# Kernel tuning notes

Hardware: AMD Instinct MI355X
Metric: run time of the kernel (lower is better)

The kernel has to match this reference:

```python
import jax, jax.numpy as jnp
import numpy as np

N_CAT, N_NUM, N_EMB, N_ENG = 53, 47, 1352, 100
E, H, FF, NEXP, NL = 128, 4, 256, 5, 6
B, L = 512, 51
EPS = 1e-5

def _ln(x, w, b):
    m = jnp.mean(x, axis=-1, keepdims=True)
    v = jnp.mean((x - m) ** 2, axis=-1, keepdims=True)
    return (x - m) * jax.lax.rsqrt(v + EPS) * w + b

def setup_inputs() -> dict:
    key = jax.random.key(0)
    ks = jax.random.split(key, 24)
    s = 0.02
    emb = jax.random.normal(ks[0], (N_EMB + 2, E), jnp.float32) * s
    emb = emb.at[0].set(0.0)  # padding_idx=0
    emb_eng = jax.random.normal(ks[1], (N_ENG, E), jnp.float32) * s
    emb_eng = emb_eng.at[0].set(0.0)
    inp = {
        'x_cat': jax.random.randint(ks[2], (B, L, N_CAT), 0, 1306, jnp.int32),
        'x_num': jax.random.normal(ks[3], (B, L, N_NUM), jnp.float32),
        'x_engineered': jax.random.normal(ks[4], (B, N_ENG), jnp.float32),
        'emb': emb,
        'emb_bias': jax.random.normal(ks[5], (N_CAT + N_NUM, E), jnp.float32),
        'emb_eng': emb_eng,
        'emb_bias_eng': jax.random.normal(ks[6], (N_ENG, E), jnp.float32),
        'ln0_w': jnp.ones((E,), jnp.float32), 'ln0_b': jnp.zeros((E,), jnp.float32),
        'ln1_w': jnp.ones((NL, E), jnp.float32), 'ln1_b': jnp.zeros((NL, E), jnp.float32),
        'Wqkv': jax.random.normal(ks[7], (NL, 3 * E, E), jnp.float32) * s,
        'bqkv': jnp.zeros((NL, 3 * E), jnp.float32),
        'Wo': jax.random.normal(ks[8], (NL, E, E), jnp.float32) * s,
        'bo': jnp.zeros((NL, E), jnp.float32),
        'ln2_w': jnp.ones((NL, E), jnp.float32), 'ln2_b': jnp.zeros((NL, E), jnp.float32),
        'Wg': jax.random.normal(ks[9], (NL, E, NEXP), jnp.float32) * s,
        'bg': jnp.zeros((NL, NEXP), jnp.float32),
        'W1': jax.random.normal(ks[10], (NL, NEXP, E, FF), jnp.float32) * s,
        'b1': jnp.zeros((NL, NEXP, FF), jnp.float32),
        'W2': jax.random.normal(ks[11], (NL, NEXP, FF, E), jnp.float32) * s,
        'b2': jnp.zeros((NL, NEXP, E), jnp.float32),
    }
    return inp

def _forward(x_cat, x_num, x_engineered, emb, emb_bias, emb_eng, emb_bias_eng,
             ln0_w, ln0_b, ln1_w, ln1_b, Wqkv, bqkv, Wo, bo,
             ln2_w, ln2_b, Wg, bg, W1, b1, W2, b2):
    b = x_cat.shape[0]
    # last order
    cat_last = x_cat[:, -1, :]                     # [B, N_CAT]
    num_last = x_num[:, -1, :]                     # [B, N_NUM]
    x_cat_emb = emb[cat_last] + emb_bias[:N_CAT][None]          # [B, N_CAT, E]
    num_idx = jnp.arange(N_EMB - N_NUM + 1, N_EMB + 1)           # rows 1306..1352
    x_num_emb = emb[num_idx][None] * num_last[..., None] + emb_bias[N_CAT:][None]
    eng_emb = emb_eng[None] * x_engineered[..., None] + emb_bias_eng[None]
    dummy = jnp.zeros((b, 1, E), x_cat_emb.dtype)
    x = jnp.concatenate([x_cat_emb, x_num_emb, eng_emb, dummy], axis=1)  # [B, 201, E]
    x = _ln(x, ln0_w, ln0_b)
    hd = E // H
    scale = 1.0 / np.sqrt(hd)
    for i in range(NL):
        # pre-norm multi-head self-attention
        h = _ln(x, ln1_w[i], ln1_b[i])
        qkv = h @ Wqkv[i].T + bqkv[i]              # [B, N, 3E]
        q, k, v = jnp.split(qkv, 3, axis=-1)
        q = q.reshape(b, -1, H, hd); k = k.reshape(b, -1, H, hd); v = v.reshape(b, -1, H, hd)
        scores = jnp.einsum('bqhd,bkhd->bhqk', q, k) * scale
        attn = jax.nn.softmax(scores, axis=-1)
        o = jnp.einsum('bhqk,bkhd->bqhd', attn, v).reshape(b, -1, E)
        x = x + o @ Wo[i].T + bo[i]
        # pre-norm MoE feedforward (dense soft mixture over experts)
        h = _ln(x, ln2_w[i], ln2_b[i])
        gate = jax.nn.softmax(h @ Wg[i] + bg[i], axis=-1)        # [B, N, NEXP]
        hid = jax.nn.relu(jnp.einsum('bne,xef->bnxf', h, W1[i]) + b1[i])
        eo = jnp.einsum('bnxf,xfe->bnxe', hid, W2[i]) + b2[i]
        x = x + jnp.einsum('bnxe,bnx->bne', eo, gate)
    return x[:, -1, :]                              # [B, E]

def reference(x_cat, x_num, x_engineered, emb, emb_bias, emb_eng, emb_bias_eng,
              ln0_w, ln0_b, ln1_w, ln1_b, Wqkv, bqkv, Wo, bo,
              ln2_w, ln2_b, Wg, bg, W1, b1, W2, b2):
    return _forward(x_cat, x_num, x_engineered, emb, emb_bias, emb_eng, emb_bias_eng,
                    ln0_w, ln0_b, ln1_w, ln1_b, Wqkv, bqkv, Wo, bo,
                    ln2_w, ln2_b, Wg, bg, W1, b1, W2, b2)
```

## Files before the change

### kernel.cpp

```cpp
#include <hip/hip_runtime.h>
#include <math.h>

#define NTOK 201
#define EDIM 128
#define LDX  132
#define NHEAD 4
#define HD   32
#define NLAY 6
#define NEXP 5
#define FFD  256
#define NCAT 53
#define NNUM 47
#define NENG 100
#define NEMB 1352
#define SEQL 51
#define NB   512
#define LN_EPS 1e-5f
#define SCALE 0.17677669529663687f

typedef __attribute__((ext_vector_type(8))) short bfrag;
typedef __attribute__((ext_vector_type(4))) float f32x4;
typedef __attribute__((ext_vector_type(8))) unsigned short u16x8;
typedef __attribute__((ext_vector_type(4))) unsigned short u16x4;

__device__ __forceinline__ float bf2f(unsigned short u){ return __uint_as_float(((unsigned)u)<<16); }
__device__ __forceinline__ unsigned short f2bf(float f){
  unsigned u = __float_as_uint(f);
  return (unsigned short)((u + 0x7FFFu + ((u>>16)&1u)) >> 16);
}

#define OFF_WQH  0u
#define OFF_WQL  589824u
#define OFF_BQ   1179648u
#define OFF_WOH  1188864u
#define OFF_WOL  1385472u
#define OFF_W1H  1582080u
#define OFF_W1L  3548160u
#define OFF_W2H  5514240u
#define OFF_W2L  7480320u

__global__ void prep_qkv_bf(const float* __restrict__ Wqkv, const float* __restrict__ bqkv,
                            unsigned short* __restrict__ Wqh, unsigned short* __restrict__ Wql,
                            float* __restrict__ bq){
  int bid = blockIdx.x; int n = bid % 384; int e = threadIdx.x;
  float sc = (n < 128) ? SCALE : 1.0f;
  float w = Wqkv[(size_t)bid*128 + e] * sc;
  unsigned short h = f2bf(w), l = f2bf(w - bf2f(h));
  Wqh[(size_t)bid*128 + e] = h; Wql[(size_t)bid*128 + e] = l;
  if (e == 0) bq[bid] = bqkv[bid] * sc;
}

__global__ void prep_wo_bf(const float* __restrict__ Wo,
                           unsigned short* __restrict__ Woh, unsigned short* __restrict__ Wol){
  int idx = blockIdx.x*blockDim.x + threadIdx.x;
  if (idx >= 6*128*128) return;
  float w = Wo[idx];
  unsigned short h = f2bf(w), l = f2bf(w - bf2f(h));
  Woh[idx] = h; Wol[idx] = l;
}

__global__ void prep_moe(const float* __restrict__ W1, const float* __restrict__ W2,
                         unsigned short* __restrict__ W1h, unsigned short* __restrict__ W1l,
                         unsigned short* __restrict__ W2h, unsigned short* __restrict__ W2l){
  const int Ntot = 6*5*128*256;
  for (int idx = blockIdx.x*blockDim.x + threadIdx.x; idx < Ntot; idx += gridDim.x*blockDim.x){
    int lx = idx / 32768; int rem = idx & 32767; int e = rem >> 8; int f = rem & 255;
    float w = W1[idx];
    unsigned short h = f2bf(w); unsigned short l = f2bf(w - bf2f(h));
    size_t o1 = (size_t)(lx*256+f)*128 + e;
    W1h[o1] = h; W1l[o1] = l;
    int f2 = (idx >> 7) & 255; int e2 = idx & 127;
    float w2 = W2[idx];
    unsigned short h2 = f2bf(w2); unsigned short l2 = f2bf(w2 - bf2f(h2));
    size_t o2 = (size_t)(lx*128+e2)*256 + f2;
    W2h[o2] = h2; W2l[o2] = l2;
  }
}

struct Params {
  const int*   x_cat;
  const float* x_num;
  const float* x_eng;
  const float* emb;
  const float* emb_bias;
  const float* emb_eng;
  const float* emb_bias_eng;
  const float* ln0w; const float* ln0b;
  const float* ln1w; const float* ln1b;
  const float* ln2w; const float* ln2b;
  const float* bo;
  const float* Wg;   const float* bg;
  const float* b1;   const float* b2;
  const unsigned short* Wqh; const unsigned short* Wql; const float* bq;
  const unsigned short* Woh; const unsigned short* Wol;
  const unsigned short* W1h; const unsigned short* W1l;
  const unsigned short* W2h; const unsigned short* W2l;
  float* out;
};

__device__ __forceinline__ void ln_stats(const float* xs, float* s_m, float* s_r, int tid){
  if (tid < NTOK){
    const float* row = xs + tid*LDX;
    float s0=0,s1=0,s2=0,s3=0;
    for (int e=0;e<EDIM;e+=4){ s0+=row[e]; s1+=row[e+1]; s2+=row[e+2]; s3+=row[e+3]; }
    float m = (s0+s1+s2+s3)*(1.0f/EDIM);
    float v0=0,v1=0,v2=0,v3=0;
    for (int e=0;e<EDIM;e+=4){
      float d0=row[e]-m,d1=row[e+1]-m,d2=row[e+2]-m,d3=row[e+3]-m;
      v0+=d0*d0; v1+=d1*d1; v2+=d2*d2; v3+=d3*d3;
    }
    s_m[tid]=m; s_r[tid]=1.0f/sqrtf((v0+v1+v2+v3)*(1.0f/EDIM)+LN_EPS);
  }
}

__global__ __launch_bounds__(512) __attribute__((amdgpu_waves_per_eu(2,2)))
void fam_fwd(Params p){
  __shared__ float xs[NTOK*LDX];
  __shared__ float s_m[NTOK], s_r[NTOK];
  __shared__ __align__(16) char scb[55296];

  const int b = blockIdx.x, tid = threadIdx.x;
  const int lane = tid & 63, wv = tid >> 6;

  {
    const int e = tid & 127, tl = tid >> 7;
    for (int t = tl; t < NTOK; t += 4){
      float v;
      if (t < NCAT){
        int idx = p.x_cat[b*(SEQL*NCAT) + (SEQL-1)*NCAT + t];
        v = p.emb[idx*EDIM+e] + p.emb_bias[t*EDIM+e];
      } else if (t < NCAT+NNUM){
        int j = t - NCAT;
        float nv = p.x_num[b*(SEQL*NNUM)+(SEQL-1)*NNUM+j];
        v = p.emb[(NEMB-NNUM+1+j)*EDIM+e]*nv + p.emb_bias[(NCAT+j)*EDIM+e];
      } else if (t < NCAT+NNUM+NENG){
        int j = t - (NCAT+NNUM);
        float ev = p.x_eng[b*NENG+j];
        v = p.emb_eng[j*EDIM+e]*ev + p.emb_bias_eng[j*EDIM+e];
      } else v = 0.f;
      xs[t*LDX+e] = v;
    }
  }
  __syncthreads();
  ln_stats(xs, s_m, s_r, tid);
  __syncthreads();
  {
    const int e = tid & 127, tl = tid >> 7;
    for (int t = tl; t < NTOK; t += 4){
      float m = s_m[t], r = s_r[t];
      xs[t*LDX+e] = (xs[t*LDX+e]-m)*r*p.ln0w[e] + p.ln0b[e];
    }
  }
  __syncthreads();

  unsigned short* Kh  = (unsigned short*)scb;
  unsigned short* Vt  = (unsigned short*)(scb + 17920);
  unsigned short* HTh = (unsigned short*)(scb + 32768);
  unsigned short* HTl = (unsigned short*)(scb + 32768 + 8704);
  unsigned short* Sb  = (unsigned short*)(scb + 32768);
  unsigned short* Ob  = (unsigned short*)(scb + 32768 + 14848);
  unsigned short* Qmh = (unsigned short*)(scb + 50176);
  unsigned short* Qml = (unsigned short*)(scb + 52736);
  float* red  = (float*)(scb + 52736);
  float* mrow = (float*)(scb + 52736 + 1056);
  float* dsum = (float*)(scb + 52736 + 1184);
  unsigned short* Ahi = (unsigned short*)scb;
  unsigned short* Alo = (unsigned short*)(scb + 8192);
  unsigned short* Hh  = (unsigned short*)(scb + 16384);
  unsigned short* Hl  = (unsigned short*)(scb + 32768);
  float*          gateb = (float*)(scb + 49152);

  for (int li = 0; li < NLAY; ++li){
    const float* ln1w = p.ln1w + li*EDIM;
    const float* ln1b = p.ln1b + li*EDIM;
    const float* ln2w = p.ln2w + li*EDIM;
    const float* ln2b = p.ln2b + li*EDIM;
    const float* bo   = p.bo + li*EDIM;
    const float* Wg   = p.Wg + li*EDIM*NEXP;
    const float* bg   = p.bg + li*NEXP;
    const float* b1g  = p.b1 + li*NEXP*FFD;
    const float* b2g  = p.b2 + li*NEXP*EDIM;

    ln_stats(xs, s_m, s_r, tid);
    __syncthreads();

    f32x4 accW[7][2];
#pragma unroll
    for (int mt=0; mt<7; ++mt){ accW[mt][0]=(f32x4){0,0,0,0}; accW[mt][1]=(f32x4){0,0,0,0}; }

    const int mfw = wv & 1;
    const int ngw = wv >> 1;

    for (int h = 0; h < NHEAD; ++h){
      {
        int sel = ngw;
        int nrow = ((sel < 2) ? (128 + h*HD + sel*16) : (256 + h*HD + (sel-2)*16)) + (lane & 15);
        const unsigned short* Bh = p.Wqh + ((size_t)li*384 + nrow)*128 + 8*(lane>>4);
        const unsigned short* Bl = p.Wql + ((size_t)li*384 + nrow)*128 + 8*(lane>>4);
        bfrag wbh[4], wbl[4];
#pragma unroll
        for (int kf=0; kf<4; ++kf){ wbh[kf] = *(const bfrag*)(Bh + kf*32); wbl[kf] = *(const bfrag*)(Bl + kf*32); }
        float bias = p.bq[li*384 + nrow];

        for (int mt=0; mt<7; ++mt){
          {
            int row = tid >> 4, c8 = (tid & 15) << 3;
            int t = mt*32 + row;
            union { unsigned short u[8]; u16x8 v; } hu, lu;
            if (t < NTOK){
              float m = s_m[t], r = s_r[t];
              const float* xr = &xs[t*LDX + c8];
              float4 a = *(const float4*)xr, b4 = *(const float4*)(xr+4);
              float4 w0 = *(const float4*)(ln1w + c8), w1 = *(const float4*)(ln1w + c8 + 4);
              float4 q0 = *(const float4*)(ln1b + c8), q1 = *(const float4*)(ln1b + c8 + 4);
              float vv[8] = {(a.x-m)*r*w0.x+q0.x,(a.y-m)*r*w0.y+q0.y,(a.z-m)*r*w0.z+q0.z,(a.w-m)*r*w0.w+q0.w,
                             (b4.x-m)*r*w1.x+q1.x,(b4.y-m)*r*w1.y+q1.y,(b4.z-m)*r*w1.z+q1.z,(b4.w-m)*r*w1.w+q1.w};
#pragma unroll
              for (int j2=0;j2<8;++j2){ unsigned short hb=f2bf(vv[j2]); hu.u[j2]=hb; lu.u[j2]=f2bf(vv[j2]-bf2f(hb)); }
            } else {
#pragma unroll
              for (int j2=0;j2<8;++j2){ hu.u[j2]=0; lu.u[j2]=0; }
            }
            *(u16x8*)(HTh + row*136 + c8) = hu.v;
            *(u16x8*)(HTl + row*136 + c8) = lu.v;
          }
          __syncthreads();
          {
            f32x4 acc = (f32x4){0,0,0,0};
#pragma unroll
            for (int kf=0; kf<4; ++kf){
              const unsigned short* ab = HTh + (mfw*16 + (lane&15))*136 + kf*32 + 8*(lane>>4);
              const unsigned short* al = HTl + (mfw*16 + (lane&15))*136 + kf*32 + 8*(lane>>4);
              bfrag ah = *(const bfrag*)ab, av = *(const bfrag*)al;
              acc = __builtin_amdgcn_mfma_f32_16x16x32_bf16(ah, wbh[kf], acc, 0,0,0);
              acc = __builtin_amdgcn_mfma_f32_16x16x32_bf16(ah, wbl[kf], acc, 0,0,0);
              acc = __builtin_amdgcn_mfma_f32_16x16x32_bf16(av, wbh[kf], acc, 0,0,0);
            }
            int col = lane & 15;
            if (sel < 2){
              int d = sel*16 + col;
#pragma unroll
              for (int reg=0; reg<4; ++reg){
                int tok = mt*32 + mfw*16 + 4*(lane>>4) + reg;
                Kh[tok*40 + d] = f2bf(acc[reg] + bias);
              }
            } else {
              int d = (sel-2)*16 + col;
              int tokb = mt*32 + mfw*16 + 4*(lane>>4);
              u16x4 pk;
#pragma unroll
              for (int reg=0; reg<4; ++reg) pk[reg] = f2bf(acc[reg] + bias);
              *(u16x4*)(Vt + d*232 + tokb) = pk;
            }
          }
          __syncthreads();
        }
      }

      bfrag wobh[2], wobl[2];
#pragma unroll
      for (int i=0;i<2;++i){
        int j = (ngw + 4*i)*16 + (lane&15);
        const unsigned short* wb = p.Woh + ((size_t)li*128 + j)*128 + h*HD + 8*(lane>>4);
        const unsigned short* wl = p.Wol + ((size_t)li*128 + j)*128 + h*HD + 8*(lane>>4);
        wobh[i] = *(const bfrag*)wb; wobl[i] = *(const bfrag*)wl;
      }

#pragma unroll
      for (int mt=0; mt<7; ++mt){
        {
          int row = tid >> 4, c8 = (tid & 15) << 3;
          int t = mt*32 + row;
          union { unsigned short u[8]; u16x8 v; } hu, lu;
          if (t < NTOK){
            float m = s_m[t], r = s_r[t];
            const float* xr = &xs[t*LDX + c8];
            float4 a = *(const float4*)xr, b4 = *(const float4*)(xr+4);
            float4 w0 = *(const float4*)(ln1w + c8), w1 = *(const float4*)(ln1w + c8 + 4);
            float4 q0 = *(const float4*)(ln1b + c8), q1 = *(const float4*)(ln1b + c8 + 4);
            float vv[8] = {(a.x-m)*r*w0.x+q0.x,(a.y-m)*r*w0.y+q0.y,(a.z-m)*r*w0.z+q0.z,(a.w-m)*r*w0.w+q0.w,
                           (b4.x-m)*r*w1.x+q1.x,(b4.y-m)*r*w1.y+q1.y,(b4.z-m)*r*w1.z+q1.z,(b4.w-m)*r*w1.w+q1.w};
#pragma unroll
            for (int j2=0;j2<8;++j2){ unsigned short hb=f2bf(vv[j2]); hu.u[j2]=hb; lu.u[j2]=f2bf(vv[j2]-bf2f(hb)); }
          } else {
#pragma unroll
            for (int j2=0;j2<8;++j2){ hu.u[j2]=0; lu.u[j2]=0; }
          }
          *(u16x8*)(HTh + row*136 + c8) = hu.v;
          *(u16x8*)(HTl + row*136 + c8) = lu.v;
        }
        __syncthreads();

        if (wv < 4){
          int mf2 = wv & 1, nf = (wv >> 1) & 1;
          int nrow = h*HD + nf*16 + (lane & 15);
          const unsigned short* Bh = p.Wqh + ((size_t)li*384 + nrow)*128 + 8*(lane>>4);
          const unsigned short* Bl = p.Wql + ((size_t)li*384 + nrow)*128 + 8*(lane>>4);
          f32x4 acc = (f32x4){0,0,0,0};
#pragma unroll
          for (int kf=0; kf<4; ++kf){
            bfrag ah = *(const bfrag*)(HTh + (mf2*16 + (lane&15))*136 + kf*32 + 8*(lane>>4));
            bfrag av = *(const bfrag*)(HTl + (mf2*16 + (lane&15))*136 + kf*32 + 8*(lane>>4));
            bfrag bh = *(const bfrag*)(Bh + kf*32);
            bfrag bl = *(const bfrag*)(Bl + kf*32);
            acc = __builtin_amdgcn_mfma_f32_16x16x32_bf16(ah, bh, acc, 0,0,0);
            acc = __builtin_amdgcn_mfma_f32_16x16x32_bf16(ah, bl, acc, 0,0,0);
            acc = __builtin_amdgcn_mfma_f32_16x16x32_bf16(av, bh, acc, 0,0,0);
          }
          float bias = p.bq[li*384 + nrow];
          int d = nf*16 + (lane & 15);
#pragma unroll
          for (int reg=0; reg<4; ++reg){
            float v = acc[reg] + bias;
            unsigned short hb = f2bf(v);
            int qrow = mf2*16 + 4*(lane>>4) + reg;
            Qmh[qrow*40 + d] = hb;
            Qml[qrow*40 + d] = f2bf(v - bf2f(hb));
          }
        }
        __syncthreads();

        {
          bfrag qh = *(const bfrag*)(Qmh + (mfw*16 + (lane&15))*40 + 8*(lane>>4));
          bfrag ql = *(const bfrag*)(Qml + (mfw*16 + (lane&15))*40 + 8*(lane>>4));
          for (int nf = ngw; nf < 14; nf += 4){
            bfrag kb = *(const bfrag*)(Kh + (nf*16 + (lane&15))*40 + 8*(lane>>4));
            f32x4 s = (f32x4){0,0,0,0};
            s = __builtin_amdgcn_mfma_f32_16x16x32_bf16(qh, kb, s, 0,0,0);
            s = __builtin_amdgcn_mfma_f32_16x16x32_bf16(ql, kb, s, 0,0,0);
            int tok = nf*16 + (lane & 15);
#pragma unroll
            for (int reg=0; reg<4; ++reg){
              int q = mfw*16 + 4*(lane>>4) + reg;
              Sb[q*232 + tok] = f2bf(s[reg]);
            }
          }
        }
        __syncthreads();

        {
          int q = tid & 31, kg = tid >> 5;
          float pmax = -INFINITY;
#pragma unroll
          for (int j2=0; j2<14; ++j2){
            int k = kg + 16*j2;
            if (k < NTOK) pmax = fmaxf(pmax, bf2f(Sb[q*232 + k]));
          }
          pmax = fmaxf(pmax, __shfl_xor(pmax, 32));
          if (!(tid & 32)) red[(tid>>6)*33 + q] = pmax;
        }
        __syncthreads();
        if (tid < 32){
          float m = red[tid];
#pragma unroll
          for (int w=1; w<8; ++w) m = fmaxf(m, red[w*33 + tid]);
          mrow[tid] = m;
        }
        __syncthreads();

        {
          int q = tid & 31, kg = tid >> 5;
          float mr = mrow[q];
          float psum = 0.f;
#pragma unroll
          for (int j2=0; j2<14; ++j2){
            int k = kg + 16*j2;
            float pe = 0.f;
            if (k < NTOK) pe = __expf(bf2f(Sb[q*232 + k]) - mr);
            psum += pe;
            Sb[q*232 + k] = f2bf(pe);
          }
          psum += __shfl_xor(psum, 32);
          if (!(tid & 32)) red[(tid>>6)*33 + q] = psum;
        }
        __syncthreads();
        if (tid < 32){
          float s = red[tid];
#pragma unroll
          for (int w=1; w<8; ++w) s += red[w*33 + tid];
          dsum[tid] = s;
        }
        __syncthreads();

        if (wv < 4){
          int mf2 = wv & 1, nf = (wv >> 1) & 1;
          f32x4 o = (f32x4){0,0,0,0};
#pragma unroll
          for (int kf=0; kf<7; ++kf){
            bfrag pa = *(const bfrag*)(Sb + (mf2*16 + (lane&15))*232 + kf*32 + 8*(lane>>4));
            bfrag vb = *(const bfrag*)(Vt + (nf*16 + (lane&15))*232 + kf*32 + 8*(lane>>4));
            o = __builtin_amdgcn_mfma_f32_16x16x32_bf16(pa, vb, o, 0,0,0);
          }
          int d = nf*16 + (lane & 15);
#pragma unroll
          for (int reg=0; reg<4; ++reg){
            int q = mf2*16 + 4*(lane>>4) + reg;
            Ob[q*40 + d] = f2bf(o[reg] * (1.0f/dsum[q]));
          }
        }
        __syncthreads();

        {
          bfrag oa = *(const bfrag*)(Ob + (mfw*16 + (lane&15))*40 + 8*(lane>>4));
          accW[mt][0] = __builtin_amdgcn_mfma_f32_16x16x32_bf16(oa, wobh[0], accW[mt][0], 0,0,0);
          accW[mt][0] = __builtin_amdgcn_mfma_f32_16x16x32_bf16(oa, wobl[0], accW[mt][0], 0,0,0);
          accW[mt][1] = __builtin_amdgcn_mfma_f32_16x16x32_bf16(oa, wobh[1], accW[mt][1], 0,0,0);
          accW[mt][1] = __builtin_amdgcn_mfma_f32_16x16x32_bf16(oa, wobl[1], accW[mt][1], 0,0,0);
        }
        __syncthreads();
      }
    }

    {
#pragma unroll
      for (int i=0;i<2;++i){
        int j = (ngw + 4*i)*16 + (lane & 15);
        float boj = bo[j];
#pragma unroll
        for (int mt=0; mt<7; ++mt){
#pragma unroll
          for (int reg=0; reg<4; ++reg){
            int t = mt*32 + mfw*16 + 4*(lane>>4) + reg;
            if (t < NTOK) xs[t*LDX + j] += accW[mt][i][reg] + boj;
          }
        }
      }
    }
    __syncthreads();

    ln_stats(xs, s_m, s_r, tid);
    __syncthreads();

    if (tid < NTOK){
      const float* row = xs + tid*LDX;
      float m = s_m[tid], r = s_r[tid];
      float gl[NEXP];
#pragma unroll
      for (int x=0;x<NEXP;++x) gl[x] = bg[x];
      for (int e=0;e<EDIM;++e){
        float hv = (row[e]-m)*r*ln2w[e] + ln2b[e];
#pragma unroll
        for (int x=0;x<NEXP;++x) gl[x] += hv*Wg[e*NEXP+x];
      }
      float gm = gl[0];
#pragma unroll
      for (int x=1;x<NEXP;++x) gm = fmaxf(gm, gl[x]);
      float gs = 0.f;
#pragma unroll
      for (int x=0;x<NEXP;++x){ gl[x] = __expf(gl[x]-gm); gs += gl[x]; }
      float gi = 1.0f/gs;
#pragma unroll
      for (int x=0;x<NEXP;++x) gateb[tid*NEXP+x] = gl[x]*gi;
    }
    __syncthreads();

    for (int t0 = 0; t0 < NTOK; t0 += 32){
      {
        int mf = tid >> 8;
        int row = (tid & 15) + 16*mf;
        int kb  = ((tid>>6)&3)*32 + 8*((tid>>4)&3);
        int t = t0 + row;
        union { unsigned short u[8]; bfrag v; } hu, lu;
        if (t < NTOK){
          float m = s_m[t], r = s_r[t];
          const float* xr = &xs[t*LDX + kb];
          float4 a = *(const float4*)xr;
          float4 bq4 = *(const float4*)(xr+4);
          float4 w0 = *(const float4*)(ln2w + kb);
          float4 w1 = *(const float4*)(ln2w + kb + 4);
          float4 bb0 = *(const float4*)(ln2b + kb);
          float4 bb1 = *(const float4*)(ln2b + kb + 4);
          float vv[8] = {(a.x-m)*r*w0.x+bb0.x, (a.y-m)*r*w0.y+bb0.y,
                         (a.z-m)*r*w0.z+bb0.z, (a.w-m)*r*w0.w+bb0.w,
                         (bq4.x-m)*r*w1.x+bb1.x, (bq4.y-m)*r*w1.y+bb1.y,
                         (bq4.z-m)*r*w1.z+bb1.z, (bq4.w-m)*r*w1.w+bb1.w};
#pragma unroll
          for (int j=0;j<8;++j){
            unsigned short hb = f2bf(vv[j]);
            hu.u[j] = hb;
            lu.u[j] = f2bf(vv[j] - bf2f(hb));
          }
        } else {
#pragma unroll
          for (int j=0;j<8;++j){ hu.u[j]=0; lu.u[j]=0; }
        }
        *(bfrag*)(Ahi + tid*8) = hu.v;
        *(bfrag*)(Alo + tid*8) = lu.v;
      }
      __syncthreads();

      f32x4 acc2[2];
      acc2[0] = (f32x4){0.f,0.f,0.f,0.f};
      acc2[1] = (f32x4){0.f,0.f,0.f,0.f};

      for (int x = 0; x < NEXP; ++x){
        const unsigned short* W1hx = p.W1h + (size_t)(li*NEXP+x)*FFD*EDIM;
        const unsigned short* W1lx = p.W1l + (size_t)(li*NEXP+x)*FFD*EDIM;
        const unsigned short* W2hx = p.W2h + (size_t)(li*NEXP+x)*EDIM*FFD;
        const unsigned short* W2lx = p.W2l + (size_t)(li*NEXP+x)*EDIM*FFD;

        f32x4 acc1[2][2];
#pragma unroll
        for (int i=0;i<2;++i){ acc1[i][0]=(f32x4){0,0,0,0}; acc1[i][1]=(f32x4){0,0,0,0}; }
#pragma unroll
        for (int kf=0;kf<4;++kf){
          bfrag ah[2], al[2], bh[2], bl[2];
#pragma unroll
          for (int mf=0;mf<2;++mf){
            ah[mf] = *(const bfrag*)(Ahi + ((mf*4+kf)*64 + lane)*8);
            al[mf] = *(const bfrag*)(Alo + ((mf*4+kf)*64 + lane)*8);
          }
#pragma unroll
          for (int nfl=0;nfl<2;++nfl){
            size_t n = (size_t)((wv*2+nfl)*16 + (lane&15));
            size_t off = n*128 + kf*32 + 8*(lane>>4);
            bh[nfl] = *(const bfrag*)(W1hx + off);
            bl[nfl] = *(const bfrag*)(W1lx + off);
          }
#pragma unroll
          for (int mf=0;mf<2;++mf)
#pragma unroll
            for (int nfl=0;nfl<2;++nfl){
              acc1[mf][nfl] = __builtin_amdgcn_mfma_f32_16x16x32_bf16(ah[mf], bh[nfl], acc1[mf][nfl], 0,0,0);
              acc1[mf][nfl] = __builtin_amdgcn_mfma_f32_16x16x32_bf16(ah[mf], bl[nfl], acc1[mf][nfl], 0,0,0);
              acc1[mf][nfl] = __builtin_amdgcn_mfma_f32_16x16x32_bf16(al[mf], bh[nfl], acc1[mf][nfl], 0,0,0);
            }
        }
        {
          int c = lane & 15;
#pragma unroll
          for (int nfl=0;nfl<2;++nfl){
            int n = (wv*2+nfl)*16 + c;
            float bb = b1g[x*FFD + n];
            int lane_t_base = 16*(2*nfl + (c>>3));
            int jcol = c & 7;
#pragma unroll
            for (int mf=0;mf<2;++mf){
#pragma unroll
              for (int reg=0;reg<4;++reg){
                int msub = (lane>>4)*4 + reg;
                int t = t0 + mf*16 + msub;
                float g = (t < NTOK) ? gateb[t*NEXP+x] : 0.f;
                float v = fmaxf(acc1[mf][nfl][reg] + bb, 0.f) * g;
                unsigned short hb = f2bf(v);
                unsigned short lb = f2bf(v - bf2f(hb));
                int idx = ((mf*8 + wv)*64 + msub + lane_t_base)*8 + jcol;
                Hh[idx] = hb; Hl[idx] = lb;
              }
            }
          }
        }
        __syncthreads();

#pragma unroll
        for (int kf=0;kf<8;++kf){
          bfrag hh[2], hl[2];
#pragma unroll
          for (int mf=0;mf<2;++mf){
            hh[mf] = *(const bfrag*)(Hh + ((mf*8+kf)*64 + lane)*8);
            hl[mf] = *(const bfrag*)(Hl + ((mf*8+kf)*64 + lane)*8);
          }
          size_t off = (size_t)(wv*16 + (lane&15))*256 + kf*32 + 8*(lane>>4);
          bfrag wh = *(const bfrag*)(W2hx + off);
          bfrag wl = *(const bfrag*)(W2lx + off);
#pragma unroll
          for (int mf=0;mf<2;++mf){
            acc2[mf] = __builtin_amdgcn_mfma_f32_16x16x32_bf16(hh[mf], wh, acc2[mf], 0,0,0);
            acc2[mf] = __builtin_amdgcn_mfma_f32_16x16x32_bf16(hh[mf], wl, acc2[mf], 0,0,0);
            acc2[mf] = __builtin_amdgcn_mfma_f32_16x16x32_bf16(hl[mf], wh, acc2[mf], 0,0,0);
          }
        }
        __syncthreads();
      }

      {
        int c = lane & 15;
        int n = wv*16 + c;
#pragma unroll
        for (int mf=0;mf<2;++mf){
#pragma unroll
          for (int reg=0;reg<4;++reg){
            int t = t0 + mf*16 + (lane>>4)*4 + reg;
            if (t < NTOK){
              float bs = 0.f;
#pragma unroll
              for (int x=0;x<NEXP;++x) bs += gateb[t*NEXP+x]*b2g[x*EDIM+n];
              xs[t*LDX+n] += acc2[mf][reg] + bs;
            }
          }
        }
      }
      __syncthreads();
    }
  }

  if (tid < EDIM) p.out[b*EDIM + tid] = xs[200*LDX + tid];
}

extern "C" void kernel_launch(void* const* d_in, const int* in_sizes, int n_in,
                              void* d_out, int out_size, void* d_ws, size_t ws_size,
                              hipStream_t stream) {
  (void)in_sizes; (void)n_in; (void)out_size; (void)ws_size;
  char* ws = (char*)d_ws;

  const float* Wqkv = (const float*)d_in[11];
  const float* bqkv = (const float*)d_in[12];
  const float* Wo   = (const float*)d_in[13];
  const float* W1   = (const float*)d_in[19];
  const float* W2   = (const float*)d_in[21];

  hipLaunchKernelGGL(prep_qkv_bf, dim3(6*384), dim3(128), 0, stream,
                     Wqkv, bqkv,
                     (unsigned short*)(ws+OFF_WQH), (unsigned short*)(ws+OFF_WQL),
                     (float*)(ws+OFF_BQ));
  hipLaunchKernelGGL(prep_wo_bf, dim3(384), dim3(256), 0, stream, Wo,
                     (unsigned short*)(ws+OFF_WOH), (unsigned short*)(ws+OFF_WOL));
  hipLaunchKernelGGL(prep_moe, dim3(3840), dim3(256), 0, stream, W1, W2,
                     (unsigned short*)(ws+OFF_W1H), (unsigned short*)(ws+OFF_W1L),
                     (unsigned short*)(ws+OFF_W2H), (unsigned short*)(ws+OFF_W2L));

  Params p;
  p.x_cat        = (const int*)  d_in[0];
  p.x_num        = (const float*)d_in[1];
  p.x_eng        = (const float*)d_in[2];
  p.emb          = (const float*)d_in[3];
  p.emb_bias     = (const float*)d_in[4];
  p.emb_eng      = (const float*)d_in[5];
  p.emb_bias_eng = (const float*)d_in[6];
  p.ln0w = (const float*)d_in[7];  p.ln0b = (const float*)d_in[8];
  p.ln1w = (const float*)d_in[9];  p.ln1b = (const float*)d_in[10];
  p.ln2w = (const float*)d_in[15]; p.ln2b = (const float*)d_in[16];
  p.bo   = (const float*)d_in[14];
  p.Wg   = (const float*)d_in[17]; p.bg = (const float*)d_in[18];
  p.b1   = (const float*)d_in[20]; p.b2 = (const float*)d_in[22];
  p.Wqh = (const unsigned short*)(ws+OFF_WQH);
  p.Wql = (const unsigned short*)(ws+OFF_WQL);
  p.bq  = (const float*)(ws+OFF_BQ);
  p.Woh = (const unsigned short*)(ws+OFF_WOH);
  p.Wol = (const unsigned short*)(ws+OFF_WOL);
  p.W1h = (const unsigned short*)(ws+OFF_W1H);
  p.W1l = (const unsigned short*)(ws+OFF_W1L);
  p.W2h = (const unsigned short*)(ws+OFF_W2H);
  p.W2l = (const unsigned short*)(ws+OFF_W2L);
  p.out = (float*)d_out;

  hipLaunchKernelGGL(fam_fwd, dim3(NB), dim3(512), 0, stream, p);
}
```

Measured before the change: 5.539 ms.

## Double block size to 1024 threads and split MFMA accumulators for ILP

Launches 1024 threads per block (16 waves) instead of 512, redistributing QKV, attention, Wo and MoE FFN work so each wave handles fewer output tiles. It also splits each MFMA accumulation chain into two interleaved accumulators summed at the end, to shorten dependency chains. The aim is more latency hiding per block, given the LDS footprint limits blocks per CU. In exchange, register budget per thread shrinks, some phases leave half the waves idle (e.g. QKV and PV use only 8 or 4 waves), and block-wide barriers now synchronize more waves.

```diff
diff --git a/kernel.cpp b/kernel.cpp
--- a/kernel.cpp
+++ b/kernel.cpp
@@ -113,8 +113,31 @@
   }
 }
 
-__global__ __launch_bounds__(512) __attribute__((amdgpu_waves_per_eu(2,2)))
-void fam_fwd(Params p){
+__device__ __forceinline__ void stage_ht(const float* xs, const float* s_m, const float* s_r,
+                                         unsigned short* HTh, unsigned short* HTl,
+                                         const float* lw, const float* lb, int t0, int tid){
+  int row = tid >> 5;
+  int c4  = (tid & 31) << 2;
+  int t = t0 + row;
+  u16x4 hu = (u16x4){0,0,0,0}, lu = (u16x4){0,0,0,0};
+  if (t < NTOK){
+    float m = s_m[t], r = s_r[t];
+    float4 a  = *(const float4*)(&xs[t*LDX + c4]);
+    float4 w  = *(const float4*)(lw + c4);
+    float4 bb = *(const float4*)(lb + c4);
+    float v0 = (a.x-m)*r*w.x + bb.x;
+    float v1 = (a.y-m)*r*w.y + bb.y;
+    float v2 = (a.z-m)*r*w.z + bb.z;
+    float v3 = (a.w-m)*r*w.w + bb.w;
+    unsigned short h0=f2bf(v0), h1=f2bf(v1), h2=f2bf(v2), h3=f2bf(v3);
+    hu = (u16x4){h0,h1,h2,h3};
+    lu = (u16x4){f2bf(v0-bf2f(h0)), f2bf(v1-bf2f(h1)), f2bf(v2-bf2f(h2)), f2bf(v3-bf2f(h3))};
+  }
+  *(u16x4*)(HTh + row*136 + c4) = hu;
+  *(u16x4*)(HTl + row*136 + c4) = lu;
+}
+
+__global__ __launch_bounds__(1024, 4) void fam_fwd(Params p){
   __shared__ float xs[NTOK*LDX];
   __shared__ float s_m[NTOK], s_r[NTOK];
   __shared__ __align__(16) char scb[55296];
@@ -124,7 +147,7 @@
 
   {
     const int e = tid & 127, tl = tid >> 7;
-    for (int t = tl; t < NTOK; t += 4){
+    for (int t = tl; t < NTOK; t += 8){
       float v;
       if (t < NCAT){
         int idx = p.x_cat[b*(SEQL*NCAT) + (SEQL-1)*NCAT + t];
@@ -146,7 +169,7 @@
   __syncthreads();
   {
     const int e = tid & 127, tl = tid >> 7;
-    for (int t = tl; t < NTOK; t += 4){
+    for (int t = tl; t < NTOK; t += 8){
       float m = s_m[t], r = s_r[t];
       xs[t*LDX+e] = (xs[t*LDX+e]-m)*r*p.ln0w[e] + p.ln0b[e];
     }
@@ -162,8 +185,8 @@
   unsigned short* Qmh = (unsigned short*)(scb + 50176);
   unsigned short* Qml = (unsigned short*)(scb + 52736);
   float* red  = (float*)(scb + 52736);
-  float* mrow = (float*)(scb + 52736 + 1056);
-  float* dsum = (float*)(scb + 52736 + 1184);
+  float* mrow = (float*)(scb + 52736 + 2112);
+  float* dsum = (float*)(scb + 52736 + 2240);
   unsigned short* Ahi = (unsigned short*)scb;
   unsigned short* Alo = (unsigned short*)(scb + 8192);
   unsigned short* Hh  = (unsigned short*)(scb + 16384);
@@ -184,130 +207,103 @@
     ln_stats(xs, s_m, s_r, tid);
     __syncthreads();
 
-    f32x4 accW[7][2];
-#pragma unroll
-    for (int mt=0; mt<7; ++mt){ accW[mt][0]=(f32x4){0,0,0,0}; accW[mt][1]=(f32x4){0,0,0,0}; }
+    f32x4 accW[7];
+#pragma unroll
+    for (int mt=0; mt<7; ++mt) accW[mt]=(f32x4){0,0,0,0};
 
     const int mfw = wv & 1;
     const int ngw = wv >> 1;
 
     for (int h = 0; h < NHEAD; ++h){
-      {
-        int sel = ngw;
+      bfrag wbh[4], wbl[4]; float bias1 = 0.f;
+      if (wv < 8){
+        int sel = wv >> 1;
         int nrow = ((sel < 2) ? (128 + h*HD + sel*16) : (256 + h*HD + (sel-2)*16)) + (lane & 15);
         const unsigned short* Bh = p.Wqh + ((size_t)li*384 + nrow)*128 + 8*(lane>>4);
         const unsigned short* Bl = p.Wql + ((size_t)li*384 + nrow)*128 + 8*(lane>>4);
-        bfrag wbh[4], wbl[4];
 #pragma unroll
         for (int kf=0; kf<4; ++kf){ wbh[kf] = *(const bfrag*)(Bh + kf*32); wbl[kf] = *(const bfrag*)(Bl + kf*32); }
-        float bias = p.bq[li*384 + nrow];
-
-        for (int mt=0; mt<7; ++mt){
-          {
-            int row = tid >> 4, c8 = (tid & 15) << 3;
-            int t = mt*32 + row;
-            union { unsigned short u[8]; u16x8 v; } hu, lu;
-            if (t < NTOK){
-              float m = s_m[t], r = s_r[t];
-              const float* xr = &xs[t*LDX + c8];
-              float4 a = *(const float4*)xr, b4 = *(const float4*)(xr+4);
-              float4 w0 = *(const float4*)(ln1w + c8), w1 = *(const float4*)(ln1w + c8 + 4);
-              float4 q0 = *(const float4*)(ln1b + c8), q1 = *(const float4*)(ln1b + c8 + 4);
-              float vv[8] = {(a.x-m)*r*w0.x+q0.x,(a.y-m)*r*w0.y+q0.y,(a.z-m)*r*w0.z+q0.z,(a.w-m)*r*w0.w+q0.w,
-                             (b4.x-m)*r*w1.x+q1.x,(b4.y-m)*r*w1.y+q1.y,(b4.z-m)*r*w1.z+q1.z,(b4.w-m)*r*w1.w+q1.w};
-#pragma unroll
-              for (int j2=0;j2<8;++j2){ unsigned short hb=f2bf(vv[j2]); hu.u[j2]=hb; lu.u[j2]=f2bf(vv[j2]-bf2f(hb)); }
+        bias1 = p.bq[li*384 + nrow];
+      }
+
+      for (int mt=0; mt<7; ++mt){
+        stage_ht(xs, s_m, s_r, HTh, HTl, ln1w, ln1b, mt*32, tid);
+        __syncthreads();
+        if (wv < 8){
+          int sel = wv >> 1, mf1 = wv & 1;
+          f32x4 aA = (f32x4){0,0,0,0}, aB = (f32x4){0,0,0,0};
+#pragma unroll
+          for (int kf=0; kf<4; ++kf){
+            bfrag ah = *(const bfrag*)(HTh + (mf1*16 + (lane&15))*136 + kf*32 + 8*(lane>>4));
+            bfrag av = *(const bfrag*)(HTl + (mf1*16 + (lane&15))*136 + kf*32 + 8*(lane>>4));
+            if (kf & 1){
+              aB = __builtin_amdgcn_mfma_f32_16x16x32_bf16(ah, wbh[kf], aB, 0,0,0);
+              aB = __builtin_amdgcn_mfma_f32_16x16x32_bf16(ah, wbl[kf], aB, 0,0,0);
+              aB = __builtin_amdgcn_mfma_f32_16x16x32_bf16(av, wbh[kf], aB, 0,0,0);
             } else {
-#pragma unroll
-              for (int j2=0;j2<8;++j2){ hu.u[j2]=0; lu.u[j2]=0; }
+              aA = __builtin_amdgcn_mfma_f32_16x16x32_bf16(ah, wbh[kf], aA, 0,0,0);
+              aA = __builtin_amdgcn_mfma_f32_16x16x32_bf16(ah, wbl[kf], aA, 0,0,0);
+              aA = __builtin_amdgcn_mfma_f32_16x16x32_bf16(av, wbh[kf], aA, 0,0,0);
             }
-            *(u16x8*)(HTh + row*136 + c8) = hu.v;
-            *(u16x8*)(HTl + row*136 + c8) = lu.v;
-          }
-          __syncthreads();
-          {
-            f32x4 acc = (f32x4){0,0,0,0};
-#pragma unroll
-            for (int kf=0; kf<4; ++kf){
-              const unsigned short* ab = HTh + (mfw*16 + (lane&15))*136 + kf*32 + 8*(lane>>4);
-              const unsigned short* al = HTl + (mfw*16 + (lane&15))*136 + kf*32 + 8*(lane>>4);
-              bfrag ah = *(const bfrag*)ab, av = *(const bfrag*)al;
-              acc = __builtin_amdgcn_mfma_f32_16x16x32_bf16(ah, wbh[kf], acc, 0,0,0);
-              acc = __builtin_amdgcn_mfma_f32_16x16x32_bf16(ah, wbl[kf], acc, 0,0,0);
-              acc = __builtin_amdgcn_mfma_f32_16x16x32_bf16(av, wbh[kf], acc, 0,0,0);
+          }
+          f32x4 acc = aA + aB;
+          int col = lane & 15;
+          if (sel < 2){
+            int d = sel*16 + col;
+#pragma unroll
+            for (int reg=0; reg<4; ++reg){
+              int tok = mt*32 + mf1*16 + 4*(lane>>4) + reg;
+              Kh[tok*40 + d] = f2bf(acc[reg] + bias1);
             }
-            int col = lane & 15;
-            if (sel < 2){
-              int d = sel*16 + col;
-#pragma unroll
-              for (int reg=0; reg<4; ++reg){
-                int tok = mt*32 + mfw*16 + 4*(lane>>4) + reg;
-                Kh[tok*40 + d] = f2bf(acc[reg] + bias);
-              }
-            } else {
-              int d = (sel-2)*16 + col;
-              int tokb = mt*32 + mfw*16 + 4*(lane>>4);
-              u16x4 pk;
-#pragma unroll
-              for (int reg=0; reg<4; ++reg) pk[reg] = f2bf(acc[reg] + bias);
-              *(u16x4*)(Vt + d*232 + tokb) = pk;
-            }
-          }
-          __syncthreads();
-        }
-      }
-
-      bfrag wobh[2], wobl[2];
-#pragma unroll
-      for (int i=0;i<2;++i){
-        int j = (ngw + 4*i)*16 + (lane&15);
+          } else {
+            int d = (sel-2)*16 + col;
+            int tokb = mt*32 + mf1*16 + 4*(lane>>4);
+            u16x4 pk;
+#pragma unroll
+            for (int reg=0; reg<4; ++reg) pk[reg] = f2bf(acc[reg] + bias1);
+            *(u16x4*)(Vt + d*232 + tokb) = pk;
+          }
+        }
+        __syncthreads();
+      }
+
+      bfrag wobh, wobl;
+      {
+        int j = ngw*16 + (lane&15);
         const unsigned short* wb = p.Woh + ((size_t)li*128 + j)*128 + h*HD + 8*(lane>>4);
         const unsigned short* wl = p.Wol + ((size_t)li*128 + j)*128 + h*HD + 8*(lane>>4);
-        wobh[i] = *(const bfrag*)wb; wobl[i] = *(const bfrag*)wl;
+        wobh = *(const bfrag*)wb; wobl = *(const bfrag*)wl;
       }
 
 #pragma unroll
       for (int mt=0; mt<7; ++mt){
-        {
-          int row = tid >> 4, c8 = (tid & 15) << 3;
-          int t = mt*32 + row;
-          union { unsigned short u[8]; u16x8 v; } hu, lu;
-          if (t < NTOK){
-            float m = s_m[t], r = s_r[t];
-            const float* xr = &xs[t*LDX + c8];
-            float4 a = *(const float4*)xr, b4 = *(const float4*)(xr+4);
-            float4 w0 = *(const float4*)(ln1w + c8), w1 = *(const float4*)(ln1w + c8 + 4);
-            float4 q0 = *(const float4*)(ln1b + c8), q1 = *(const float4*)(ln1b + c8 + 4);
-            float vv[8] = {(a.x-m)*r*w0.x+q0.x,(a.y-m)*r*w0.y+q0.y,(a.z-m)*r*w0.z+q0.z,(a.w-m)*r*w0.w+q0.w,
-                           (b4.x-m)*r*w1.x+q1.x,(b4.y-m)*r*w1.y+q1.y,(b4.z-m)*r*w1.z+q1.z,(b4.w-m)*r*w1.w+q1.w};
-#pragma unroll
-            for (int j2=0;j2<8;++j2){ unsigned short hb=f2bf(vv[j2]); hu.u[j2]=hb; lu.u[j2]=f2bf(vv[j2]-bf2f(hb)); }
-          } else {
-#pragma unroll
-            for (int j2=0;j2<8;++j2){ hu.u[j2]=0; lu.u[j2]=0; }
-          }
-          *(u16x8*)(HTh + row*136 + c8) = hu.v;
-          *(u16x8*)(HTl + row*136 + c8) = lu.v;
-        }
+        stage_ht(xs, s_m, s_r, HTh, HTl, ln1w, ln1b, mt*32, tid);
         __syncthreads();
 
         if (wv < 4){
-          int mf2 = wv & 1, nf = (wv >> 1) & 1;
+          int mf2 = wv & 1, nf = wv >> 1;
           int nrow = h*HD + nf*16 + (lane & 15);
           const unsigned short* Bh = p.Wqh + ((size_t)li*384 + nrow)*128 + 8*(lane>>4);
           const unsigned short* Bl = p.Wql + ((size_t)li*384 + nrow)*128 + 8*(lane>>4);
-          f32x4 acc = (f32x4){0,0,0,0};
+          f32x4 aA = (f32x4){0,0,0,0}, aB = (f32x4){0,0,0,0};
 #pragma unroll
           for (int kf=0; kf<4; ++kf){
             bfrag ah = *(const bfrag*)(HTh + (mf2*16 + (lane&15))*136 + kf*32 + 8*(lane>>4));
             bfrag av = *(const bfrag*)(HTl + (mf2*16 + (lane&15))*136 + kf*32 + 8*(lane>>4));
             bfrag bh = *(const bfrag*)(Bh + kf*32);
             bfrag bl = *(const bfrag*)(Bl + kf*32);
-            acc = __builtin_amdgcn_mfma_f32_16x16x32_bf16(ah, bh, acc, 0,0,0);
-            acc = __builtin_amdgcn_mfma_f32_16x16x32_bf16(ah, bl, acc, 0,0,0);
-            acc = __builtin_amdgcn_mfma_f32_16x16x32_bf16(av, bh, acc, 0,0,0);
-          }
-          float bias = p.bq[li*384 + nrow];
+            if (kf & 1){
+              aB = __builtin_amdgcn_mfma_f32_16x16x32_bf16(ah, bh, aB, 0,0,0);
+              aB = __builtin_amdgcn_mfma_f32_16x16x32_bf16(ah, bl, aB, 0,0,0);
+              aB = __builtin_amdgcn_mfma_f32_16x16x32_bf16(av, bh, aB, 0,0,0);
+            } else {
+              aA = __builtin_amdgcn_mfma_f32_16x16x32_bf16(ah, bh, aA, 0,0,0);
+              aA = __builtin_amdgcn_mfma_f32_16x16x32_bf16(ah, bl, aA, 0,0,0);
+              aA = __builtin_amdgcn_mfma_f32_16x16x32_bf16(av, bh, aA, 0,0,0);
+            }
+          }
+          f32x4 acc = aA + aB;
+          float bias = p.bq[li*384 + h*HD + nf*16 + (lane&15)];
           int d = nf*16 + (lane & 15);
 #pragma unroll
           for (int reg=0; reg<4; ++reg){
@@ -323,16 +319,20 @@
         {
           bfrag qh = *(const bfrag*)(Qmh + (mfw*16 + (lane&15))*40 + 8*(lane>>4));
           bfrag ql = *(const bfrag*)(Qml + (mfw*16 + (lane&15))*40 + 8*(lane>>4));
-          for (int nf = ngw; nf < 14; nf += 4){
-            bfrag kb = *(const bfrag*)(Kh + (nf*16 + (lane&15))*40 + 8*(lane>>4));
-            f32x4 s = (f32x4){0,0,0,0};
-            s = __builtin_amdgcn_mfma_f32_16x16x32_bf16(qh, kb, s, 0,0,0);
-            s = __builtin_amdgcn_mfma_f32_16x16x32_bf16(ql, kb, s, 0,0,0);
-            int tok = nf*16 + (lane & 15);
-#pragma unroll
-            for (int reg=0; reg<4; ++reg){
-              int q = mfw*16 + 4*(lane>>4) + reg;
-              Sb[q*232 + tok] = f2bf(s[reg]);
+#pragma unroll
+          for (int rep=0; rep<2; ++rep){
+            int nf = ngw + 8*rep;
+            if (nf < 14){
+              bfrag kb = *(const bfrag*)(Kh + (nf*16 + (lane&15))*40 + 8*(lane>>4));
+              f32x4 s = (f32x4){0,0,0,0};
+              s = __builtin_amdgcn_mfma_f32_16x16x32_bf16(qh, kb, s, 0,0,0);
+              s = __builtin_amdgcn_mfma_f32_16x16x32_bf16(ql, kb, s, 0,0,0);
+              int tok = nf*16 + (lane & 15);
+#pragma unroll
+              for (int reg=0; reg<4; ++reg){
+                int q = mfw*16 + 4*(lane>>4) + reg;
+                Sb[q*232 + tok] = f2bf(s[reg]);
+              }
             }
           }
         }
@@ -342,18 +342,18 @@
           int q = tid & 31, kg = tid >> 5;
           float pmax = -INFINITY;
 #pragma unroll
-          for (int j2=0; j2<14; ++j2){
-            int k = kg + 16*j2;
+          for (int j2=0; j2<7; ++j2){
+            int k = kg + 32*j2;
             if (k < NTOK) pmax = fmaxf(pmax, bf2f(Sb[q*232 + k]));
           }
           pmax = fmaxf(pmax, __shfl_xor(pmax, 32));
-          if (!(tid & 32)) red[(tid>>6)*33 + q] = pmax;
+          if (!(tid & 32)) red[wv*33 + q] = pmax;
         }
         __syncthreads();
         if (tid < 32){
           float m = red[tid];
 #pragma unroll
-          for (int w=1; w<8; ++w) m = fmaxf(m, red[w*33 + tid]);
+          for (int w=1; w<16; ++w) m = fmaxf(m, red[w*33 + tid]);
           mrow[tid] = m;
         }
         __syncthreads();
@@ -363,34 +363,36 @@
           float mr = mrow[q];
           float psum = 0.f;
 #pragma unroll
-          for (int j2=0; j2<14; ++j2){
-            int k = kg + 16*j2;
+          for (int j2=0; j2<7; ++j2){
+            int k = kg + 32*j2;
             float pe = 0.f;
             if (k < NTOK) pe = __expf(bf2f(Sb[q*232 + k]) - mr);
             psum += pe;
             Sb[q*232 + k] = f2bf(pe);
           }
           psum += __shfl_xor(psum, 32);
-          if (!(tid & 32)) red[(tid>>6)*33 + q] = psum;
+          if (!(tid & 32)) red[wv*33 + q] = psum;
         }
         __syncthreads();
         if (tid < 32){
           float s = red[tid];
 #pragma unroll
-          for (int w=1; w<8; ++w) s += red[w*33 + tid];
+          for (int w=1; w<16; ++w) s += red[w*33 + tid];
           dsum[tid] = s;
         }
         __syncthreads();
 
         if (wv < 4){
-          int mf2 = wv & 1, nf = (wv >> 1) & 1;
-          f32x4 o = (f32x4){0,0,0,0};
+          int mf2 = wv & 1, nf = wv >> 1;
+          f32x4 oA = (f32x4){0,0,0,0}, oB = (f32x4){0,0,0,0};
 #pragma unroll
           for (int kf=0; kf<7; ++kf){
             bfrag pa = *(const bfrag*)(Sb + (mf2*16 + (lane&15))*232 + kf*32 + 8*(lane>>4));
             bfrag vb = *(const bfrag*)(Vt + (nf*16 + (lane&15))*232 + kf*32 + 8*(lane>>4));
-            o = __builtin_amdgcn_mfma_f32_16x16x32_bf16(pa, vb, o, 0,0,0);
-          }
+            if (kf & 1) oB = __builtin_amdgcn_mfma_f32_16x16x32_bf16(pa, vb, oB, 0,0,0);
+            else        oA = __builtin_amdgcn_mfma_f32_16x16x32_bf16(pa, vb, oA, 0,0,0);
+          }
+          f32x4 o = oA + oB;
           int d = nf*16 + (lane & 15);
 #pragma unroll
           for (int reg=0; reg<4; ++reg){
@@ -402,27 +404,22 @@
 
         {
           bfrag oa = *(const bfrag*)(Ob + (mfw*16 + (lane&15))*40 + 8*(lane>>4));
-          accW[mt][0] = __builtin_amdgcn_mfma_f32_16x16x32_bf16(oa, wobh[0], accW[mt][0], 0,0,0);
-          accW[mt][0] = __builtin_amdgcn_mfma_f32_16x16x32_bf16(oa, wobl[0], accW[mt][0], 0,0,0);
-          accW[mt][1] = __builtin_amdgcn_mfma_f32_16x16x32_bf16(oa, wobh[1], accW[mt][1], 0,0,0);
-          accW[mt][1] = __builtin_amdgcn_mfma_f32_16x16x32_bf16(oa, wobl[1], accW[mt][1], 0,0,0);
+          accW[mt] = __builtin_amdgcn_mfma_f32_16x16x32_bf16(oa, wobh, accW[mt], 0,0,0);
+          accW[mt] = __builtin_amdgcn_mfma_f32_16x16x32_bf16(oa, wobl, accW[mt], 0,0,0);
         }
         __syncthreads();
       }
     }
 
     {
-#pragma unroll
-      for (int i=0;i<2;++i){
-        int j = (ngw + 4*i)*16 + (lane & 15);
-        float boj = bo[j];
-#pragma unroll
-        for (int mt=0; mt<7; ++mt){
-#pragma unroll
-          for (int reg=0; reg<4; ++reg){
-            int t = mt*32 + mfw*16 + 4*(lane>>4) + reg;
-            if (t < NTOK) xs[t*LDX + j] += accW[mt][i][reg] + boj;
-          }
+      int j = ngw*16 + (lane & 15);
+      float boj = bo[j];
+#pragma unroll
+      for (int mt=0; mt<7; ++mt){
+#pragma unroll
+        for (int reg=0; reg<4; ++reg){
+          int t = mt*32 + mfw*16 + 4*(lane>>4) + reg;
+          if (t < NTOK) xs[t*LDX + j] += accW[mt][reg] + boj;
         }
       }
     }
@@ -454,8 +451,9 @@
     }
     __syncthreads();
 
+    const int mfg = wv >> 3, nfg = wv & 7;
     for (int t0 = 0; t0 < NTOK; t0 += 32){
-      {
+      if (tid < 512){
         int mf = tid >> 8;
         int row = (tid & 15) + 16*mf;
         int kb  = ((tid>>6)&3)*32 + 8*((tid>>4)&3);
@@ -489,9 +487,7 @@
       }
       __syncthreads();
 
-      f32x4 acc2[2];
-      acc2[0] = (f32x4){0.f,0.f,0.f,0.f};
-      acc2[1] = (f32x4){0.f,0.f,0.f,0.f};
+      f32x4 a2a = (f32x4){0,0,0,0}, a2b = (f32x4){0,0,0,0};
 
       for (int x = 0; x < NEXP; ++x){
         const unsigned short* W1hx = p.W1h + (size_t)(li*NEXP+x)*FFD*EDIM;
@@ -499,54 +495,51 @@
         const unsigned short* W2hx = p.W2h + (size_t)(li*NEXP+x)*EDIM*FFD;
         const unsigned short* W2lx = p.W2l + (size_t)(li*NEXP+x)*EDIM*FFD;
 
-        f32x4 acc1[2][2];
-#pragma unroll
-        for (int i=0;i<2;++i){ acc1[i][0]=(f32x4){0,0,0,0}; acc1[i][1]=(f32x4){0,0,0,0}; }
+        f32x4 a1a[2], a1b[2];
+#pragma unroll
+        for (int i=0;i<2;++i){ a1a[i]=(f32x4){0,0,0,0}; a1b[i]=(f32x4){0,0,0,0}; }
 #pragma unroll
         for (int kf=0;kf<4;++kf){
-          bfrag ah[2], al[2], bh[2], bl[2];
+          bfrag ah[2], al[2];
 #pragma unroll
           for (int mf=0;mf<2;++mf){
             ah[mf] = *(const bfrag*)(Ahi + ((mf*4+kf)*64 + lane)*8);
             al[mf] = *(const bfrag*)(Alo + ((mf*4+kf)*64 + lane)*8);
           }
-#pragma unroll
-          for (int nfl=0;nfl<2;++nfl){
-            size_t n = (size_t)((wv*2+nfl)*16 + (lane&15));
-            size_t off = n*128 + kf*32 + 8*(lane>>4);
-            bh[nfl] = *(const bfrag*)(W1hx + off);
-            bl[nfl] = *(const bfrag*)(W1lx + off);
-          }
-#pragma unroll
-          for (int mf=0;mf<2;++mf)
-#pragma unroll
-            for (int nfl=0;nfl<2;++nfl){
-              acc1[mf][nfl] = __builtin_amdgcn_mfma_f32_16x16x32_bf16(ah[mf], bh[nfl], acc1[mf][nfl], 0,0,0);
-              acc1[mf][nfl] = __builtin_amdgcn_mfma_f32_16x16x32_bf16(ah[mf], bl[nfl], acc1[mf][nfl], 0,0,0);
-              acc1[mf][nfl] = __builtin_amdgcn_mfma_f32_16x16x32_bf16(al[mf], bh[nfl], acc1[mf][nfl], 0,0,0);
+          size_t n = (size_t)(wv*16 + (lane&15));
+          size_t off = n*128 + kf*32 + 8*(lane>>4);
+          bfrag bh = *(const bfrag*)(W1hx + off);
+          bfrag bl = *(const bfrag*)(W1lx + off);
+#pragma unroll
+          for (int mf=0;mf<2;++mf){
+            if (kf & 1){
+              a1b[mf] = __builtin_amdgcn_mfma_f32_16x16x32_bf16(ah[mf], bh, a1b[mf], 0,0,0);
+              a1b[mf] = __builtin_amdgcn_mfma_f32_16x16x32_bf16(ah[mf], bl, a1b[mf], 0,0,0);
+              a1b[mf] = __builtin_amdgcn_mfma_f32_16x16x32_bf16(al[mf], bh, a1b[mf], 0,0,0);
+            } else {
+              a1a[mf] = __builtin_amdgcn_mfma_f32_16x16x32_bf16(ah[mf], bh, a1a[mf], 0,0,0);
+              a1a[mf] = __builtin_amdgcn_mfma_f32_16x16x32_bf16(ah[mf], bl, a1a[mf], 0,0,0);
+              a1a[mf] = __builtin_amdgcn_mfma_f32_16x16x32_bf16(al[mf], bh, a1a[mf], 0,0,0);
             }
+          }
         }
         {
           int c = lane & 15;
-#pragma unroll
-          for (int nfl=0;nfl<2;++nfl){
-            int n = (wv*2+nfl)*16 + c;
-            float bb = b1g[x*FFD + n];
-            int lane_t_base = 16*(2*nfl + (c>>3));
-            int jcol = c & 7;
-#pragma unroll
-            for (int mf=0;mf<2;++mf){
-#pragma unroll
-              for (int reg=0;reg<4;++reg){
-                int msub = (lane>>4)*4 + reg;
-                int t = t0 + mf*16 + msub;
-                float g = (t < NTOK) ? gateb[t*NEXP+x] : 0.f;
-                float v = fmaxf(acc1[mf][nfl][reg] + bb, 0.f) * g;
-                unsigned short hb = f2bf(v);
-                unsigned short lb = f2bf(v - bf2f(hb));
-                int idx = ((mf*8 + wv)*64 + msub + lane_t_base)*8 + jcol;
-                Hh[idx] = hb; Hl[idx] = lb;
-              }
+          int n = wv*16 + c;
+          float bb = b1g[x*FFD + n];
+#pragma unroll
+          for (int mf=0;mf<2;++mf){
+            f32x4 s = a1a[mf] + a1b[mf];
+#pragma unroll
+            for (int reg=0;reg<4;++reg){
+              int msub = (lane>>4)*4 + reg;
+              int t = t0 + mf*16 + msub;
+              float g = (t < NTOK) ? gateb[t*NEXP+x] : 0.f;
+              float v = fmaxf(s[reg] + bb, 0.f) * g;
+              unsigned short hb = f2bf(v);
+              unsigned short lb = f2bf(v - bf2f(hb));
+              int idx = ((mf*8 + (n>>5))*64 + msub + 16*((n>>3)&3))*8 + (n&7);
+              Hh[idx] = hb; Hl[idx] = lb;
             }
           }
         }
@@ -554,20 +547,19 @@
 
 #pragma unroll
         for (int kf=0;kf<8;++kf){
-          bfrag hh[2], hl[2];
-#pragma unroll
-          for (int mf=0;mf<2;++mf){
-            hh[mf] = *(const bfrag*)(Hh + ((mf*8+kf)*64 + lane)*8);
-            hl[mf] = *(const bfrag*)(Hl + ((mf*8+kf)*64 + lane)*8);
-          }
-          size_t off = (size_t)(wv*16 + (lane&15))*256 + kf*32 + 8*(lane>>4);
+          bfrag hh = *(const bfrag*)(Hh + ((mfg*8+kf)*64 + lane)*8);
+          bfrag hl = *(const bfrag*)(Hl + ((mfg*8+kf)*64 + lane)*8);
+          size_t off = (size_t)(nfg*16 + (lane&15))*256 + kf*32 + 8*(lane>>4);
           bfrag wh = *(const bfrag*)(W2hx + off);
           bfrag wl = *(const bfrag*)(W2lx + off);
-#pragma unroll
-          for (int mf=0;mf<2;++mf){
-            acc2[mf] = __builtin_amdgcn_mfma_f32_16x16x32_bf16(hh[mf], wh, acc2[mf], 0,0,0);
-            acc2[mf] = __builtin_amdgcn_mfma_f32_16x16x32_bf16(hh[mf], wl, acc2[mf], 0,0,0);
-            acc2[mf] = __builtin_amdgcn_mfma_f32_16x16x32_bf16(hl[mf], wh, acc2[mf], 0,0,0);
+          if (kf & 1){
+            a2b = __builtin_amdgcn_mfma_f32_16x16x32_bf16(hh, wh, a2b, 0,0,0);
+            a2b = __builtin_amdgcn_mfma_f32_16x16x32_bf16(hh, wl, a2b, 0,0,0);
+            a2b = __builtin_amdgcn_mfma_f32_16x16x32_bf16(hl, wh, a2b, 0,0,0);
+          } else {
+            a2a = __builtin_amdgcn_mfma_f32_16x16x32_bf16(hh, wh, a2a, 0,0,0);
+            a2a = __builtin_amdgcn_mfma_f32_16x16x32_bf16(hh, wl, a2a, 0,0,0);
+            a2a = __builtin_amdgcn_mfma_f32_16x16x32_bf16(hl, wh, a2a, 0,0,0);
           }
         }
         __syncthreads();
@@ -575,18 +567,15 @@
 
       {
         int c = lane & 15;
-        int n = wv*16 + c;
-#pragma unroll
-        for (int mf=0;mf<2;++mf){
-#pragma unroll
-          for (int reg=0;reg<4;++reg){
-            int t = t0 + mf*16 + (lane>>4)*4 + reg;
-            if (t < NTOK){
-              float bs = 0.f;
-#pragma unroll
-              for (int x=0;x<NEXP;++x) bs += gateb[t*NEXP+x]*b2g[x*EDIM+n];
-              xs[t*LDX+n] += acc2[mf][reg] + bs;
-            }
+        int n = nfg*16 + c;
+#pragma unroll
+        for (int reg=0;reg<4;++reg){
+          int t = t0 + mfg*16 + (lane>>4)*4 + reg;
+          if (t < NTOK){
+            float bs = 0.f;
+#pragma unroll
+            for (int x=0;x<NEXP;++x) bs += gateb[t*NEXP+x]*b2g[x*EDIM+n];
+            xs[t*LDX+n] += a2a[reg] + a2b[reg] + bs;
           }
         }
       }
@@ -644,5 +633,5 @@
   p.W2l = (const unsigned short*)(ws+OFF_W2L);
   p.out = (float*)d_out;
 
-  hipLaunchKernelGGL(fam_fwd, dim3(NB), dim3(512), 0, stream, p);
-}
+  hipLaunchKernelGGL(fam_fwd, dim3(NB), dim3(1024), 0, stream, p);
+}
```

Result: slower. 8.094 ms (+46.1%).
